# Performance work log

Hardware: AMD Instinct MI355X
Metric: run time of the kernel (lower is better)

## Reference

```python
import jax, jax.numpy as jnp
import numpy as np

N_HEAD, DK, DV = 16, 64, 64
TEMP = DK ** 0.5
LN_EPS = 1e-5


def setup_inputs() -> dict:
    key = jax.random.key(0)
    ks = jax.random.split(key, 8)
    B, LQ, LK = 8, 1024, 1024
    D1, D2 = 768, 1024
    return {
        'q': jax.random.normal(ks[0], (B, LQ, D1), jnp.float32),
        'k': jax.random.normal(ks[1], (B, LK, D2), jnp.float32),
        'v': jax.random.normal(ks[2], (B, LK, D2), jnp.float32),
        'w_qs': jax.random.normal(ks[3], (D1, N_HEAD * DK), jnp.float32) * 0.02,
        'w_ks': jax.random.normal(ks[4], (D2, N_HEAD * DK), jnp.float32) * 0.02,
        'w_vs': jax.random.normal(ks[5], (D2, N_HEAD * DV), jnp.float32) * 0.02,
        'fc_w': jax.random.normal(ks[6], (N_HEAD * DV, D2), jnp.float32) * 0.02,
        'resid_w': jax.random.normal(ks[7], (D1, N_HEAD * DV), jnp.float32) * 0.02,
        'resid_b': jnp.zeros((N_HEAD * DV,), jnp.float32),
        'ln_gamma': jnp.ones((D2,), jnp.float32),
        'ln_beta': jnp.zeros((D2,), jnp.float32),
    }


def reference(q, k, v, w_qs, w_ks, w_vs, fc_w, resid_w, resid_b, ln_gamma, ln_beta):
    B, LQ, _ = q.shape
    LK = k.shape[1]
    residual = q
    # project and split heads: [B, L, H, d] -> [B, H, L, d]
    Q = (q @ w_qs).reshape(B, LQ, N_HEAD, DK).transpose(0, 2, 1, 3)
    K = (k @ w_ks).reshape(B, LK, N_HEAD, DK).transpose(0, 2, 1, 3)
    V = (v @ w_vs).reshape(B, LK, N_HEAD, DV).transpose(0, 2, 1, 3)
    scores = jnp.einsum('bhqd,bhkd->bhqk', Q / TEMP, K)
    p = jax.nn.softmax(scores, axis=-1)
    # reverse-complement attention (RCA): reverse=True
    p = (1.0 - p) / (LK - 1)
    out = jnp.einsum('bhqk,bhkd->bhqd', p, V)  # dropout is eval-mode identity
    out = out.transpose(0, 2, 1, 3).reshape(B, LQ, N_HEAD * DV)
    out = out @ fc_w
    out = out + (residual @ resid_w + resid_b)
    mean = jnp.mean(out, axis=-1, keepdims=True)
    var = jnp.var(out, axis=-1, keepdims=True)
    out = (out - mean) * jax.lax.rsqrt(var + LN_EPS) * ln_gamma + ln_beta
    return out  # relu=False
```

## Files before the change

kernel.cpp:

```cpp
#include <hip/hip_runtime.h>

typedef __bf16 bf16_t;
typedef __bf16 bf16x8 __attribute__((ext_vector_type(8)));
typedef __bf16 bf16x4 __attribute__((ext_vector_type(4)));
typedef float  f32x4  __attribute__((ext_vector_type(4)));

#if __has_builtin(__builtin_amdgcn_exp2f)
#define EXP2(x) __builtin_amdgcn_exp2f(x)
#else
#define EXP2(x) exp2f(x)
#endif

#define DEVFN __device__ __forceinline__

DEVFN void gl_lds16(void* lds_base, const void* gsrc) {
  __builtin_amdgcn_global_load_lds(
      (const __attribute__((address_space(1))) void*)gsrc,
      (__attribute__((address_space(3))) void*)lds_base, 16, 0, 0);
}

__global__ __launch_bounds__(256) void k_convert_all(
    const float* __restrict__ q, const float* __restrict__ k, const float* __restrict__ v,
    bf16_t* __restrict__ qb, bf16_t* __restrict__ kb, bf16_t* __restrict__ vb,
    float* __restrict__ Vs) {
  if (blockIdx.x == 0) {
    for (int j = threadIdx.x; j < 8192; j += 256) Vs[j] = 0.f;
  }
  const int NQ = 1572864, NK = 2097152, NT = NQ + 2 * NK;
  int stride = gridDim.x * 256;
  for (int i = blockIdx.x * 256 + threadIdx.x; i < NT; i += stride) {
    const float* src; bf16_t* dst; int off;
    if (i < NQ)           { src = q; dst = qb; off = i; }
    else if (i < NQ + NK) { src = k; dst = kb; off = i - NQ; }
    else                  { src = v; dst = vb; off = i - NQ - NK; }
    float4 vv = reinterpret_cast<const float4*>(src)[off];
    bf16x4 o;
    o[0] = (bf16_t)vv.x; o[1] = (bf16_t)vv.y; o[2] = (bf16_t)vv.z; o[3] = (bf16_t)vv.w;
    reinterpret_cast<bf16x4*>(dst)[off] = o;
  }
}

__global__ __launch_bounds__(256) void k_transpose_all(
    const float* __restrict__ w_qs, const float* __restrict__ w_ks,
    const float* __restrict__ w_vs, const float* __restrict__ fc_w,
    const float* __restrict__ resid_w,
    bf16_t* __restrict__ wqsT, bf16_t* __restrict__ wksT, bf16_t* __restrict__ wvsT,
    bf16_t* __restrict__ fcwT, bf16_t* __restrict__ rswT) {
  int bid = blockIdx.x;
  const float* w; bf16_t* wt; int K;
  if (bid < 192)      { w = w_qs;    wt = wqsT; K = 768; }
  else if (bid < 448) { w = w_ks;    wt = wksT; K = 1024; bid -= 192; }
  else if (bid < 704) { w = w_vs;    wt = wvsT; K = 1024; bid -= 448; }
  else if (bid < 960) { w = fc_w;    wt = fcwT; K = 1024; bid -= 704; }
  else                { w = resid_w; wt = rswT; K = 768;  bid -= 960; }
  __shared__ float t[64][65];
  const int bk = (bid >> 4) << 6;
  const int bn = (bid & 15) << 6;
  const int rr = threadIdx.x >> 4;
  const int cc = (threadIdx.x & 15) << 2;
#pragma unroll
  for (int i = 0; i < 4; ++i) {
    int r = i * 16 + rr;
    float4 v = *reinterpret_cast<const float4*>(&w[(size_t)(bk + r) * 1024 + bn + cc]);
    t[r][cc] = v.x; t[r][cc + 1] = v.y; t[r][cc + 2] = v.z; t[r][cc + 3] = v.w;
  }
  __syncthreads();
#pragma unroll
  for (int i = 0; i < 4; ++i) {
    int n = i * 16 + rr;
    bf16x4 o;
    o[0] = (bf16_t)t[cc][n];     o[1] = (bf16_t)t[cc + 1][n];
    o[2] = (bf16_t)t[cc + 2][n]; o[3] = (bf16_t)t[cc + 3][n];
    *reinterpret_cast<bf16x4*>(&wt[(size_t)(bn + n) * K + bk + cc]) = o;
  }
}

__global__ __launch_bounds__(256) void k_transpose_v(
    const bf16_t* __restrict__ Vp, bf16_t* __restrict__ Vt, float* __restrict__ Vs) {
  const int kt = blockIdx.x & 15;
  const int bh = blockIdx.x >> 4;
  const int b = bh >> 4, h = bh & 15;
  __shared__ unsigned short t[64][72];
  __shared__ float red[4][64];
#pragma unroll
  for (int i = 0; i < 2; ++i) {
    int cid = i * 256 + threadIdx.x;
    int r = cid >> 3, c = (cid & 7) * 8;
    uint4 v = *reinterpret_cast<const uint4*>(
        Vp + ((size_t)(b * 1024 + kt * 64 + r)) * 1024 + h * 64 + c);
    const unsigned short* pv = reinterpret_cast<const unsigned short*>(&v);
#pragma unroll
    for (int j = 0; j < 8; ++j) t[r][c + j] = pv[j];
  }
  __syncthreads();
#pragma unroll
  for (int i = 0; i < 2; ++i) {
    int cid = i * 256 + threadIdx.x;
    int d = cid >> 3, c = (cid & 7) * 8;
    unsigned short tmp[8];
#pragma unroll
    for (int j = 0; j < 8; ++j) tmp[j] = t[c + j][d];
    char* dst = (char*)Vt + ((size_t)(bh * 16 + kt)) * 8192 + d * 128 +
                ((((c >> 3) ^ (d & 7))) << 4);
    *reinterpret_cast<uint4*>(dst) = *reinterpret_cast<uint4*>(tmp);
  }
  const int d = threadIdx.x & 63, seg = threadIdx.x >> 6;
  float s = 0.f;
#pragma unroll
  for (int i = 0; i < 16; ++i)
    s += (float)*(const bf16_t*)&t[seg * 16 + i][d];
  red[seg][d] = s;
  __syncthreads();
  if (threadIdx.x < 64)
    atomicAdd(&Vs[bh * 64 + threadIdx.x],
              red[0][threadIdx.x] + red[1][threadIdx.x] + red[2][threadIdx.x] + red[3][threadIdx.x]);
}

DEVFN void gemm_core(const bf16_t* __restrict__ A, const bf16_t* __restrict__ Bt,
                     bf16_t* __restrict__ C, int N, int K, float oscale,
                     int wg, bf16_t (*sm)[4096]) {
  const int tn = N >> 7;
  const int m0 = (wg / tn) << 7;
  const int n0 = (wg % tn) << 7;
  const int lane = threadIdx.x & 63;
  const int wv = threadIdx.x >> 6;
  const int wr = (wv >> 1) * 64, wc = (wv & 1) * 64;
  const int lr = lane & 15, lk = lane >> 4;
  const int so0 = wv * 2048 + lane * 16;
  const int so1 = so0 + 1024;
  const int r0 = so0 >> 6, c0 = so0 & 63;
  const int r1 = so1 >> 6, c1 = so1 & 63;
  const char* Apc = (const char*)A;
  const char* Btc = (const char*)Bt;
  f32x4 zro = {0.f, 0.f, 0.f, 0.f};
  f32x4 acc[4][4];
#pragma unroll
  for (int i = 0; i < 4; ++i)
#pragma unroll
    for (int j = 0; j < 4; ++j) acc[i][j] = zro;

  const int nk = K >> 5;
  auto stage = [&](int buf, int t) {
    gl_lds16((char*)sm[buf] + wv * 2048,        Apc + ((size_t)(m0 + r0) * K + t * 32) * 2 + c0);
    gl_lds16((char*)sm[buf] + wv * 2048 + 1024, Apc + ((size_t)(m0 + r1) * K + t * 32) * 2 + c1);
    gl_lds16((char*)sm[2 + buf] + wv * 2048,        Btc + ((size_t)(n0 + r0) * K + t * 32) * 2 + c0);
    gl_lds16((char*)sm[2 + buf] + wv * 2048 + 1024, Btc + ((size_t)(n0 + r1) * K + t * 32) * 2 + c1);
  };
  stage(0, 0);
  __syncthreads();
  for (int t = 0; t < nk; ++t) {
    const int cur = t & 1;
    if (t + 1 < nk) stage(cur ^ 1, t + 1);
    const char* AsB = (const char*)sm[cur];
    const char* BsB = (const char*)sm[2 + cur];
    bf16x8 af[4], bfr[4];
#pragma unroll
    for (int i = 0; i < 4; ++i)
      af[i] = *(const bf16x8*)(AsB + (wr + i * 16 + lr) * 64 + lk * 16);
#pragma unroll
    for (int j = 0; j < 4; ++j)
      bfr[j] = *(const bf16x8*)(BsB + (wc + j * 16 + lr) * 64 + lk * 16);
#pragma unroll
    for (int i = 0; i < 4; ++i)
#pragma unroll
      for (int j = 0; j < 4; ++j)
        acc[i][j] = __builtin_amdgcn_mfma_f32_16x16x32_bf16(af[i], bfr[j], acc[i][j], 0, 0, 0);
    __syncthreads();
  }
#pragma unroll
  for (int i = 0; i < 4; ++i)
#pragma unroll
    for (int j = 0; j < 4; ++j)
#pragma unroll
      for (int r = 0; r < 4; ++r)
        C[(size_t)(m0 + wr + i * 16 + lk * 4 + r) * N + n0 + wc + j * 16 + lr] =
            (bf16_t)(acc[i][j][r] * oscale);
}

__global__ __launch_bounds__(256) void k_gemm_proj(
    const bf16_t* __restrict__ qb, const bf16_t* __restrict__ wqsT, bf16_t* __restrict__ Qp,
    const bf16_t* __restrict__ kb, const bf16_t* __restrict__ wksT, bf16_t* __restrict__ Kp,
    const bf16_t* __restrict__ vb, const bf16_t* __restrict__ wvsT, bf16_t* __restrict__ Vp,
    float qscale) {
  __shared__ bf16_t sm[4][4096];
  const int bid = blockIdx.x;
  const int route = bid >> 9;
  const int sbid = bid & 511;
  const int wg = (sbid & 7) * 64 + (sbid >> 3);
  if (route == 0)      gemm_core(qb, wqsT, Qp, 1024, 768,  qscale, wg, sm);
  else if (route == 1) gemm_core(kb, wksT, Kp, 1024, 1024, 1.0f,   wg, sm);
  else                 gemm_core(vb, wvsT, Vp, 1024, 1024, 1.0f,   wg, sm);
}

__global__ __launch_bounds__(256) void k_gemm_final(
    const bf16_t* __restrict__ A1, const bf16_t* __restrict__ B1t, int K1,
    const bf16_t* __restrict__ A2, const bf16_t* __restrict__ B2t, int K2,
    const float* __restrict__ bias, float* __restrict__ Y, int N) {
  __shared__ bf16_t sm[4][4096];
  const int bpx = gridDim.x >> 3;
  const int wg = (blockIdx.x & 7) * bpx + (blockIdx.x >> 3);
  const int tn = N >> 7;
  const int m0 = (wg / tn) << 7;
  const int n0 = (wg % tn) << 7;
  const int lane = threadIdx.x & 63;
  const int wv = threadIdx.x >> 6;
  const int wr = (wv >> 1) * 64, wc = (wv & 1) * 64;
  const int lr = lane & 15, lk = lane >> 4;
  const int so0 = wv * 2048 + lane * 16;
  const int so1 = so0 + 1024;
  const int r0 = so0 >> 6, c0 = so0 & 63;
  const int r1 = so1 >> 6, c1 = so1 & 63;
  f32x4 zro = {0.f, 0.f, 0.f, 0.f};
  f32x4 acc[4][4];
#pragma unroll
  for (int i = 0; i < 4; ++i)
#pragma unroll
    for (int j = 0; j < 4; ++j) acc[i][j] = zro;

  const bf16_t* Ap[2] = {A1, A2};
  const bf16_t* Bp[2] = {B1t, B2t};
  const int Kp_[2] = {K1, K2};
  for (int ph = 0; ph < 2; ++ph) {
    const char* Apc = (const char*)Ap[ph];
    const char* Btc = (const char*)Bp[ph];
    const int K = Kp_[ph];
    const int nk = K >> 5;
    auto stage = [&](int buf, int t) {
      gl_lds16((char*)sm[buf] + wv * 2048,        Apc + ((size_t)(m0 + r0) * K + t * 32) * 2 + c0);
      gl_lds16((char*)sm[buf] + wv * 2048 + 1024, Apc + ((size_t)(m0 + r1) * K + t * 32) * 2 + c1);
      gl_lds16((char*)sm[2 + buf] + wv * 2048,        Btc + ((size_t)(n0 + r0) * K + t * 32) * 2 + c0);
      gl_lds16((char*)sm[2 + buf] + wv * 2048 + 1024, Btc + ((size_t)(n0 + r1) * K + t * 32) * 2 + c1);
    };
    stage(0, 0);
    __syncthreads();
    for (int t = 0; t < nk; ++t) {
      const int cur = t & 1;
      if (t + 1 < nk) stage(cur ^ 1, t + 1);
      const char* AsB = (const char*)sm[cur];
      const char* BsB = (const char*)sm[2 + cur];
      bf16x8 af[4], bfr[4];
#pragma unroll
      for (int i = 0; i < 4; ++i)
        af[i] = *(const bf16x8*)(AsB + (wr + i * 16 + lr) * 64 + lk * 16);
#pragma unroll
      for (int j = 0; j < 4; ++j)
        bfr[j] = *(const bf16x8*)(BsB + (wc + j * 16 + lr) * 64 + lk * 16);
#pragma unroll
      for (int i = 0; i < 4; ++i)
#pragma unroll
        for (int j = 0; j < 4; ++j)
          acc[i][j] = __builtin_amdgcn_mfma_f32_16x16x32_bf16(af[i], bfr[j], acc[i][j], 0, 0, 0);
      __syncthreads();
    }
  }
#pragma unroll
  for (int i = 0; i < 4; ++i)
#pragma unroll
    for (int j = 0; j < 4; ++j) {
      float bv = bias[n0 + wc + j * 16 + lr];
#pragma unroll
      for (int r = 0; r < 4; ++r)
        Y[(size_t)(m0 + wr + i * 16 + lk * 4 + r) * N + n0 + wc + j * 16 + lr] =
            acc[i][j][r] + bv;
    }
}

__global__ __launch_bounds__(256) void k_attn(
    const bf16_t* __restrict__ Qp, const bf16_t* __restrict__ Kp,
    const bf16_t* __restrict__ Vt, const float* __restrict__ Vsum,
    bf16_t* __restrict__ Aout) {
  const int bid = blockIdx.x;
  const int wgid = (bid & 7) * 128 + (bid >> 3);
  const int qg = wgid & 7;
  const int bh = wgid >> 3;
  const int b = bh >> 4, h = bh & 15;
  __shared__ bf16_t Ks[2][64 * 64];
  __shared__ bf16_t Vs[2][64 * 64];
  const int lane = threadIdx.x & 63;
  const int wv = threadIdx.x >> 6;
  const int lr = lane & 15, lk = lane >> 4;

  const int o0 = wv * 2048 + lane * 16;
  const int o1 = o0 + 1024;
  const int row0 = o0 >> 7, row1 = o1 >> 7;
  const int sc0 = ((((o0 >> 4) & 7) ^ (row0 & 7)) << 4);
  const int sc1 = ((((o1 >> 4) & 7) ^ (row1 & 7)) << 4);
  const int srow0 = (row0 & 0x23) | ((row0 & 0x0C) << 1) | ((row0 & 0x10) >> 2);
  const int srow1 = (row1 & 0x23) | ((row1 & 0x0C) << 1) | ((row1 & 0x10) >> 2);

  const char* Ksrc0 = (const char*)(Kp + ((size_t)(b * 1024 + srow0)) * 1024 + h * 64) + sc0;
  const char* Ksrc1 = (const char*)(Kp + ((size_t)(b * 1024 + srow1)) * 1024 + h * 64) + sc1;
  const char* Vtile = (const char*)Vt + (size_t)bh * 131072 + o0;

  gl_lds16((char*)&Ks[0][0] + o0, Ksrc0);
  gl_lds16((char*)&Ks[0][0] + o1, Ksrc1);
  gl_lds16((char*)&Vs[0][0] + o0, Vtile);
  gl_lds16((char*)&Vs[0][0] + o1, Vtile + 1024);

  bf16x8 qa[2][2];
#pragma unroll
  for (int st = 0; st < 2; ++st) {
    const char* qsrc =
        (const char*)(Qp + ((size_t)(b * 1024 + qg * 128 + st * 64 + wv * 16 + lr)) * 1024 + h * 64);
    qa[st][0] = *(const bf16x8*)(qsrc + lk * 16);
    qa[st][1] = *(const bf16x8*)(qsrc + 64 + lk * 16);
  }
  __syncthreads();

  const int kb0 = lr * 128 + ((lk ^ (lr & 7)) << 4);
  const int kb1 = lr * 128 + (((4 + lk) ^ (lr & 7)) << 4);
  const int vsw0 = lr * 128 + (((0 + lk) ^ (lr & 7)) << 4);
  const int vsw1 = lr * 128 + (((4 + lk) ^ (lr & 7)) << 4);

  f32x4 zro = {0.f, 0.f, 0.f, 0.f};
  f32x4 oacc[2][4];
  f32x4 sum[2];
#pragma unroll
  for (int st = 0; st < 2; ++st) {
    sum[st] = zro;
#pragma unroll
    for (int g = 0; g < 4; ++g) oacc[st][g] = zro;
  }
  bf16x8 ones8;
#pragma unroll
  for (int j = 0; j < 8; ++j) ones8[j] = (bf16_t)1.0f;

  for (int kt = 0; kt < 16; ++kt) {
    const int cur = kt & 1;
    const char* KsB = (const char*)&Ks[cur][0];
    const char* VsB = (const char*)&Vs[cur][0];
    if (kt < 15) {
      char* KsN = (char*)&Ks[cur ^ 1][0];
      char* VsN = (char*)&Vs[cur ^ 1][0];
      const size_t koff = (size_t)(kt + 1) * 131072;
      const size_t voff = (size_t)(kt + 1) * 8192;
      gl_lds16(KsN + o0, Ksrc0 + koff);
      gl_lds16(KsN + o1, Ksrc1 + koff);
      gl_lds16(VsN + o0, Vtile + voff);
      gl_lds16(VsN + o1, Vtile + voff + 1024);
    }

    f32x4 sacc[2][4];
#pragma unroll
    for (int st = 0; st < 2; ++st)
#pragma unroll
      for (int g = 0; g < 4; ++g) sacc[st][g] = zro;
    {
      bf16x8 kf[4];
#pragma unroll
      for (int g = 0; g < 4; ++g) kf[g] = *(const bf16x8*)(KsB + kb0 + g * 2048);
#pragma unroll
      for (int st = 0; st < 2; ++st)
#pragma unroll
        for (int g = 0; g < 4; ++g)
          sacc[st][g] = __builtin_amdgcn_mfma_f32_16x16x32_bf16(kf[g], qa[st][0], sacc[st][g], 0, 0, 0);
#pragma unroll
      for (int g = 0; g < 4; ++g) kf[g] = *(const bf16x8*)(KsB + kb1 + g * 2048);
#pragma unroll
      for (int st = 0; st < 2; ++st)
#pragma unroll
        for (int g = 0; g < 4; ++g)
          sacc[st][g] = __builtin_amdgcn_mfma_f32_16x16x32_bf16(kf[g], qa[st][1], sacc[st][g], 0, 0, 0);
    }

    bf16x8 pa[2][2];
#pragma unroll
    for (int st = 0; st < 2; ++st)
#pragma unroll
      for (int c = 0; c < 2; ++c) {
        bf16x8 pw;
#pragma unroll
        for (int r = 0; r < 4; ++r) {
          pw[r]     = (bf16_t)EXP2(sacc[st][2 * c][r]);
          pw[4 + r] = (bf16_t)EXP2(sacc[st][2 * c + 1][r]);
        }
        pa[st][c] = pw;
      }

#pragma unroll
    for (int c = 0; c < 2; ++c) {
      const int vb = (c == 0) ? vsw0 : vsw1;
      bf16x8 vf[4];
#pragma unroll
      for (int gd = 0; gd < 4; ++gd)
        vf[gd] = *(const bf16x8*)(VsB + vb + gd * 2048);
#pragma unroll
      for (int st = 0; st < 2; ++st) {
        sum[st] = __builtin_amdgcn_mfma_f32_16x16x32_bf16(pa[st][c], ones8, sum[st], 0, 0, 0);
#pragma unroll
        for (int gd = 0; gd < 4; ++gd)
          oacc[st][gd] = __builtin_amdgcn_mfma_f32_16x16x32_bf16(pa[st][c], vf[gd], oacc[st][gd], 0, 0, 0);
      }
    }
    __syncthreads();
  }

  float vs_d[4];
#pragma unroll
  for (int gd = 0; gd < 4; ++gd) vs_d[gd] = Vsum[bh * 64 + gd * 16 + lr];
#pragma unroll
  for (int st = 0; st < 2; ++st) {
    float inv[4];
#pragma unroll
    for (int r = 0; r < 4; ++r) inv[r] = 1.0f / sum[st][r];
#pragma unroll
    for (int gd = 0; gd < 4; ++gd)
#pragma unroll
      for (int r = 0; r < 4; ++r) {
        int d = gd * 16 + lr;
        int qrow = qg * 128 + st * 64 + wv * 16 + lk * 4 + r;
        float attnv = oacc[st][gd][r] * inv[r];
        float val = (vs_d[gd] - attnv) * (1.0f / 1023.0f);
        Aout[((size_t)(b * 1024 + qrow)) * 1024 + h * 64 + d] = (bf16_t)val;
      }
  }
}

__global__ __launch_bounds__(256) void k_ln(
    const float* __restrict__ Y, const float* __restrict__ gamma,
    const float* __restrict__ beta, float* __restrict__ out) {
  const int row = blockIdx.x, tid = threadIdx.x;
  const float4 x = reinterpret_cast<const float4*>(Y + (size_t)row * 1024)[tid];
  float s = x.x + x.y + x.z + x.w;
  float q = x.x * x.x + x.y * x.y + x.z * x.z + x.w * x.w;
#pragma unroll
  for (int off = 32; off > 0; off >>= 1) {
    s += __shfl_xor(s, off, 64);
    q += __shfl_xor(q, off, 64);
  }
  __shared__ float ss[4], qs[4];
  if ((tid & 63) == 0) { ss[tid >> 6] = s; qs[tid >> 6] = q; }
  __syncthreads();
  s = ss[0] + ss[1] + ss[2] + ss[3];
  q = qs[0] + qs[1] + qs[2] + qs[3];
  float mean = s * (1.f / 1024.f);
  float var = q * (1.f / 1024.f) - mean * mean;
  float rstd = rsqrtf(var + 1e-5f);
  float4 g = reinterpret_cast<const float4*>(gamma)[tid];
  float4 bt = reinterpret_cast<const float4*>(beta)[tid];
  float4 o;
  o.x = (x.x - mean) * rstd * g.x + bt.x;
  o.y = (x.y - mean) * rstd * g.y + bt.y;
  o.z = (x.z - mean) * rstd * g.z + bt.z;
  o.w = (x.w - mean) * rstd * g.w + bt.w;
  reinterpret_cast<float4*>(out + (size_t)row * 1024)[tid] = o;
}

extern "C" void kernel_launch(void* const* d_in, const int* in_sizes, int n_in,
                              void* d_out, int out_size, void* d_ws, size_t ws_size,
                              hipStream_t stream) {
  (void)in_sizes; (void)n_in; (void)out_size;
  const float* q       = (const float*)d_in[0];
  const float* k       = (const float*)d_in[1];
  const float* v       = (const float*)d_in[2];
  const float* w_qs    = (const float*)d_in[3];
  const float* w_ks    = (const float*)d_in[4];
  const float* w_vs    = (const float*)d_in[5];
  const float* fc_w    = (const float*)d_in[6];
  const float* resid_w = (const float*)d_in[7];
  const float* resid_b = (const float*)d_in[8];
  const float* ln_g    = (const float*)d_in[9];
  const float* ln_b    = (const float*)d_in[10];
  float* out = (float*)d_out;
  char* ws = (char*)d_ws;

  if (ws_size < (size_t)122716160) return;

  bf16_t* qb   = (bf16_t*)(ws + 0);
  bf16_t* kb   = (bf16_t*)(ws + 12582912);
  bf16_t* vb   = (bf16_t*)(ws + 29360128);
  float*  Y    = (float*)(ws + 12582912);
  bf16_t* wqsT = (bf16_t*)(ws + 46137344);
  bf16_t* wksT = (bf16_t*)(ws + 47710208);
  bf16_t* wvsT = (bf16_t*)(ws + 49807360);
  bf16_t* fcwT = (bf16_t*)(ws + 51904512);
  bf16_t* rswT = (bf16_t*)(ws + 54001664);
  bf16_t* Qp   = (bf16_t*)(ws + 55574528);
  bf16_t* Kp   = (bf16_t*)(ws + 72351744);
  bf16_t* Vp   = (bf16_t*)(ws + 89128960);
  bf16_t* Aout = (bf16_t*)(ws + 89128960);
  bf16_t* VtT  = (bf16_t*)(ws + 105906176);
  float*  Vsm  = (float*)(ws + 122683392);

  k_convert_all<<<2048, 256, 0, stream>>>(q, k, v, qb, kb, vb, Vsm);
  k_transpose_all<<<1152, 256, 0, stream>>>(w_qs, w_ks, w_vs, fc_w, resid_w,
                                            wqsT, wksT, wvsT, fcwT, rswT);
  k_gemm_proj<<<1536, 256, 0, stream>>>(qb, wqsT, Qp, kb, wksT, Kp, vb, wvsT, Vp,
                                        0.18033688011f);
  k_transpose_v<<<2048, 256, 0, stream>>>(Vp, VtT, Vsm);
  k_attn<<<1024, 256, 0, stream>>>(Qp, Kp, VtT, Vsm, Aout);
  k_gemm_final<<<512, 256, 0, stream>>>(Aout, fcwT, 1024, qb, rswT, 768, resid_b, Y, 1024);
  k_ln<<<8192, 256, 0, stream>>>(Y, ln_g, ln_b, out);
}
```

Baseline: 198.3 us.

## Merge prep kernels, XOR-swizzle GEMM LDS tiles, store pre-LN output as bf16

```diff
diff --git a/kernel.cpp b/kernel.cpp
--- a/kernel.cpp
+++ b/kernel.cpp
@@ -19,16 +19,52 @@
       (__attribute__((address_space(3))) void*)lds_base, 16, 0, 0);
 }
 
-__global__ __launch_bounds__(256) void k_convert_all(
+__global__ __launch_bounds__(256) void k_prep(
     const float* __restrict__ q, const float* __restrict__ k, const float* __restrict__ v,
+    const float* __restrict__ w_qs, const float* __restrict__ w_ks,
+    const float* __restrict__ w_vs, const float* __restrict__ fc_w,
+    const float* __restrict__ resid_w,
     bf16_t* __restrict__ qb, bf16_t* __restrict__ kb, bf16_t* __restrict__ vb,
+    bf16_t* __restrict__ wqsT, bf16_t* __restrict__ wksT, bf16_t* __restrict__ wvsT,
+    bf16_t* __restrict__ fcwT, bf16_t* __restrict__ rswT,
     float* __restrict__ Vs) {
-  if (blockIdx.x == 0) {
+  __shared__ float t[64][65];
+  int bid = blockIdx.x;
+  if (bid < 1152) {
+    const float* w; bf16_t* wt; int K;
+    if (bid < 192)      { w = w_qs;    wt = wqsT; K = 768; }
+    else if (bid < 448) { w = w_ks;    wt = wksT; K = 1024; bid -= 192; }
+    else if (bid < 704) { w = w_vs;    wt = wvsT; K = 1024; bid -= 448; }
+    else if (bid < 960) { w = fc_w;    wt = fcwT; K = 1024; bid -= 704; }
+    else                { w = resid_w; wt = rswT; K = 768;  bid -= 960; }
+    const int bk = (bid >> 4) << 6;
+    const int bn = (bid & 15) << 6;
+    const int rr = threadIdx.x >> 4;
+    const int cc = (threadIdx.x & 15) << 2;
+#pragma unroll
+    for (int i = 0; i < 4; ++i) {
+      int r = i * 16 + rr;
+      float4 vv = *reinterpret_cast<const float4*>(&w[(size_t)(bk + r) * 1024 + bn + cc]);
+      t[r][cc] = vv.x; t[r][cc + 1] = vv.y; t[r][cc + 2] = vv.z; t[r][cc + 3] = vv.w;
+    }
+    __syncthreads();
+#pragma unroll
+    for (int i = 0; i < 4; ++i) {
+      int n = i * 16 + rr;
+      bf16x4 o;
+      o[0] = (bf16_t)t[cc][n];     o[1] = (bf16_t)t[cc + 1][n];
+      o[2] = (bf16_t)t[cc + 2][n]; o[3] = (bf16_t)t[cc + 3][n];
+      *reinterpret_cast<bf16x4*>(&wt[(size_t)(bn + n) * K + bk + cc]) = o;
+    }
+    return;
+  }
+  bid -= 1152;
+  if (bid == 0) {
     for (int j = threadIdx.x; j < 8192; j += 256) Vs[j] = 0.f;
   }
   const int NQ = 1572864, NK = 2097152, NT = NQ + 2 * NK;
-  int stride = gridDim.x * 256;
-  for (int i = blockIdx.x * 256 + threadIdx.x; i < NT; i += stride) {
+  int stride = (gridDim.x - 1152) * 256;
+  for (int i = bid * 256 + threadIdx.x; i < NT; i += stride) {
     const float* src; bf16_t* dst; int off;
     if (i < NQ)           { src = q; dst = qb; off = i; }
     else if (i < NQ + NK) { src = k; dst = kb; off = i - NQ; }
@@ -37,41 +73,6 @@
     bf16x4 o;
     o[0] = (bf16_t)vv.x; o[1] = (bf16_t)vv.y; o[2] = (bf16_t)vv.z; o[3] = (bf16_t)vv.w;
     reinterpret_cast<bf16x4*>(dst)[off] = o;
-  }
-}
-
-__global__ __launch_bounds__(256) void k_transpose_all(
-    const float* __restrict__ w_qs, const float* __restrict__ w_ks,
-    const float* __restrict__ w_vs, const float* __restrict__ fc_w,
-    const float* __restrict__ resid_w,
-    bf16_t* __restrict__ wqsT, bf16_t* __restrict__ wksT, bf16_t* __restrict__ wvsT,
-    bf16_t* __restrict__ fcwT, bf16_t* __restrict__ rswT) {
-  int bid = blockIdx.x;
-  const float* w; bf16_t* wt; int K;
-  if (bid < 192)      { w = w_qs;    wt = wqsT; K = 768; }
-  else if (bid < 448) { w = w_ks;    wt = wksT; K = 1024; bid -= 192; }
-  else if (bid < 704) { w = w_vs;    wt = wvsT; K = 1024; bid -= 448; }
-  else if (bid < 960) { w = fc_w;    wt = fcwT; K = 1024; bid -= 704; }
-  else                { w = resid_w; wt = rswT; K = 768;  bid -= 960; }
-  __shared__ float t[64][65];
-  const int bk = (bid >> 4) << 6;
-  const int bn = (bid & 15) << 6;
-  const int rr = threadIdx.x >> 4;
-  const int cc = (threadIdx.x & 15) << 2;
-#pragma unroll
-  for (int i = 0; i < 4; ++i) {
-    int r = i * 16 + rr;
-    float4 v = *reinterpret_cast<const float4*>(&w[(size_t)(bk + r) * 1024 + bn + cc]);
-    t[r][cc] = v.x; t[r][cc + 1] = v.y; t[r][cc + 2] = v.z; t[r][cc + 3] = v.w;
-  }
-  __syncthreads();
-#pragma unroll
-  for (int i = 0; i < 4; ++i) {
-    int n = i * 16 + rr;
-    bf16x4 o;
-    o[0] = (bf16_t)t[cc][n];     o[1] = (bf16_t)t[cc + 1][n];
-    o[2] = (bf16_t)t[cc + 2][n]; o[3] = (bf16_t)t[cc + 3][n];
-    *reinterpret_cast<bf16x4*>(&wt[(size_t)(bn + n) * K + bk + cc]) = o;
   }
 }
 
@@ -128,8 +129,10 @@
   const int lr = lane & 15, lk = lane >> 4;
   const int so0 = wv * 2048 + lane * 16;
   const int so1 = so0 + 1024;
-  const int r0 = so0 >> 6, c0 = so0 & 63;
-  const int r1 = so1 >> 6, c1 = so1 & 63;
+  const int r0 = so0 >> 6, r1 = so1 >> 6;
+  const int c0 = ((((so0 >> 4) & 3) ^ (r0 & 3)) << 4);
+  const int c1 = ((((so1 >> 4) & 3) ^ (r1 & 3)) << 4);
+  const int asw = ((lk ^ (lr & 3)) << 4);
   const char* Apc = (const char*)A;
   const char* Btc = (const char*)Bt;
   f32x4 zro = {0.f, 0.f, 0.f, 0.f};
@@ -156,10 +159,10 @@
     bf16x8 af[4], bfr[4];
 #pragma unroll
     for (int i = 0; i < 4; ++i)
-      af[i] = *(const bf16x8*)(AsB + (wr + i * 16 + lr) * 64 + lk * 16);
+      af[i] = *(const bf16x8*)(AsB + (wr + i * 16 + lr) * 64 + asw);
 #pragma unroll
     for (int j = 0; j < 4; ++j)
-      bfr[j] = *(const bf16x8*)(BsB + (wc + j * 16 + lr) * 64 + lk * 16);
+      bfr[j] = *(const bf16x8*)(BsB + (wc + j * 16 + lr) * 64 + asw);
 #pragma unroll
     for (int i = 0; i < 4; ++i)
 #pragma unroll
@@ -195,7 +198,7 @@
 __global__ __launch_bounds__(256) void k_gemm_final(
     const bf16_t* __restrict__ A1, const bf16_t* __restrict__ B1t, int K1,
     const bf16_t* __restrict__ A2, const bf16_t* __restrict__ B2t, int K2,
-    const float* __restrict__ bias, float* __restrict__ Y, int N) {
+    const float* __restrict__ bias, bf16_t* __restrict__ Y, int N) {
   __shared__ bf16_t sm[4][4096];
   const int bpx = gridDim.x >> 3;
   const int wg = (blockIdx.x & 7) * bpx + (blockIdx.x >> 3);
@@ -208,8 +211,10 @@
   const int lr = lane & 15, lk = lane >> 4;
   const int so0 = wv * 2048 + lane * 16;
   const int so1 = so0 + 1024;
-  const int r0 = so0 >> 6, c0 = so0 & 63;
-  const int r1 = so1 >> 6, c1 = so1 & 63;
+  const int r0 = so0 >> 6, r1 = so1 >> 6;
+  const int c0 = ((((so0 >> 4) & 3) ^ (r0 & 3)) << 4);
+  const int c1 = ((((so1 >> 4) & 3) ^ (r1 & 3)) << 4);
+  const int asw = ((lk ^ (lr & 3)) << 4);
   f32x4 zro = {0.f, 0.f, 0.f, 0.f};
   f32x4 acc[4][4];
 #pragma unroll
@@ -241,10 +246,10 @@
       bf16x8 af[4], bfr[4];
 #pragma unroll
       for (int i = 0; i < 4; ++i)
-        af[i] = *(const bf16x8*)(AsB + (wr + i * 16 + lr) * 64 + lk * 16);
+        af[i] = *(const bf16x8*)(AsB + (wr + i * 16 + lr) * 64 + asw);
 #pragma unroll
       for (int j = 0; j < 4; ++j)
-        bfr[j] = *(const bf16x8*)(BsB + (wc + j * 16 + lr) * 64 + lk * 16);
+        bfr[j] = *(const bf16x8*)(BsB + (wc + j * 16 + lr) * 64 + asw);
 #pragma unroll
       for (int i = 0; i < 4; ++i)
 #pragma unroll
@@ -261,7 +266,7 @@
 #pragma unroll
       for (int r = 0; r < 4; ++r)
         Y[(size_t)(m0 + wr + i * 16 + lk * 4 + r) * N + n0 + wc + j * 16 + lr] =
-            acc[i][j][r] + bv;
+            (bf16_t)(acc[i][j][r] + bv);
     }
 }
 
@@ -417,12 +422,13 @@
 }
 
 __global__ __launch_bounds__(256) void k_ln(
-    const float* __restrict__ Y, const float* __restrict__ gamma,
+    const bf16_t* __restrict__ Y, const float* __restrict__ gamma,
     const float* __restrict__ beta, float* __restrict__ out) {
   const int row = blockIdx.x, tid = threadIdx.x;
-  const float4 x = reinterpret_cast<const float4*>(Y + (size_t)row * 1024)[tid];
-  float s = x.x + x.y + x.z + x.w;
-  float q = x.x * x.x + x.y * x.y + x.z * x.z + x.w * x.w;
+  bf16x4 xv = reinterpret_cast<const bf16x4*>(Y + (size_t)row * 1024)[tid];
+  float x0 = (float)xv[0], x1 = (float)xv[1], x2 = (float)xv[2], x3 = (float)xv[3];
+  float s = x0 + x1 + x2 + x3;
+  float q = x0 * x0 + x1 * x1 + x2 * x2 + x3 * x3;
 #pragma unroll
   for (int off = 32; off > 0; off >>= 1) {
     s += __shfl_xor(s, off, 64);
@@ -439,10 +445,10 @@
   float4 g = reinterpret_cast<const float4*>(gamma)[tid];
   float4 bt = reinterpret_cast<const float4*>(beta)[tid];
   float4 o;
-  o.x = (x.x - mean) * rstd * g.x + bt.x;
-  o.y = (x.y - mean) * rstd * g.y + bt.y;
-  o.z = (x.z - mean) * rstd * g.z + bt.z;
-  o.w = (x.w - mean) * rstd * g.w + bt.w;
+  o.x = (x0 - mean) * rstd * g.x + bt.x;
+  o.y = (x1 - mean) * rstd * g.y + bt.y;
+  o.z = (x2 - mean) * rstd * g.z + bt.z;
+  o.w = (x3 - mean) * rstd * g.w + bt.w;
   reinterpret_cast<float4*>(out + (size_t)row * 1024)[tid] = o;
 }
 
@@ -469,7 +475,7 @@
   bf16_t* qb   = (bf16_t*)(ws + 0);
   bf16_t* kb   = (bf16_t*)(ws + 12582912);
   bf16_t* vb   = (bf16_t*)(ws + 29360128);
-  float*  Y    = (float*)(ws + 12582912);
+  bf16_t* Y    = (bf16_t*)(ws + 12582912);
   bf16_t* wqsT = (bf16_t*)(ws + 46137344);
   bf16_t* wksT = (bf16_t*)(ws + 47710208);
   bf16_t* wvsT = (bf16_t*)(ws + 49807360);
@@ -482,9 +488,8 @@
   bf16_t* VtT  = (bf16_t*)(ws + 105906176);
   float*  Vsm  = (float*)(ws + 122683392);
 
-  k_convert_all<<<2048, 256, 0, stream>>>(q, k, v, qb, kb, vb, Vsm);
-  k_transpose_all<<<1152, 256, 0, stream>>>(w_qs, w_ks, w_vs, fc_w, resid_w,
-                                            wqsT, wksT, wvsT, fcwT, rswT);
+  k_prep<<<3200, 256, 0, stream>>>(q, k, v, w_qs, w_ks, w_vs, fc_w, resid_w,
+                                   qb, kb, vb, wqsT, wksT, wvsT, fcwT, rswT, Vsm);
   k_gemm_proj<<<1536, 256, 0, stream>>>(qb, wqsT, Qp, kb, wksT, Kp, vb, wvsT, Vp,
                                         0.18033688011f);
   k_transpose_v<<<2048, 256, 0, stream>>>(Vp, VtT, Vsm);
```

Result: no change. 195.4 us (-1.5%).
